# Kernel optimization log

Measured on AMD Instinct MI355X. Metric: run time of the kernel, lower is better.

## Reference

```python
import jax, jax.numpy as jnp
import numpy as np

EPS = 1e-5


def setup_inputs() -> dict:
    key = jax.random.key(0)
    ks = jax.random.split(key, 24)
    B, S, D = 32, 1024, 768        # batch, num_segs, feature_dim
    E, G, C, P = 2, 8, 64, 384     # expansion, groups, num_clusters, latent_clus_dim
    EF = E * D                     # 1536
    GFS = EF // G                  # group_feature_size = 192
    s = 0.02
    f32 = jnp.float32
    return {
        "x": jax.random.normal(ks[0], (B, S, D), f32),
        "W_exp": s * jax.random.normal(ks[1], (D, EF), f32),
        "b_exp": jnp.zeros((EF,), f32),
        "W_ga": s * jax.random.normal(ks[2], (EF, G), f32),
        "b_ga": jnp.zeros((G,), f32),
        "bn1_g": jnp.ones((G * C,), f32) + 0.1 * jax.random.normal(ks[3], (G * C,), f32),
        "bn1_b": 0.1 * jax.random.normal(ks[4], (G * C,), f32),
        "bn1_m": 0.05 * jax.random.normal(ks[5], (G * C,), f32),
        "bn1_v": 1.0 + 0.1 * jax.random.uniform(ks[6], (G * C,), f32),
        "cluster_weights": s * jax.random.normal(ks[7], (EF, G * C), f32),
        "W_proj": s * jax.random.normal(ks[8], (GFS, D), f32),
        "b_proj": jnp.zeros((D,), f32),
        "bn2_g": jnp.ones((C,), f32) + 0.1 * jax.random.normal(ks[9], (C,), f32),
        "bn2_b": 0.1 * jax.random.normal(ks[10], (C,), f32),
        "bn2_m": 0.05 * jax.random.normal(ks[11], (C,), f32),
        "bn2_v": 1.0 + 0.1 * jax.random.uniform(ks[12], (C,), f32),
        "Wq": s * jax.random.normal(ks[13], (D, P), f32),
        "bq": jnp.zeros((P,), f32),
        "Wkv": s * jax.random.normal(ks[14], (D, 2 * P), f32),
        "bkv": jnp.zeros((2 * P,), f32),
        "Wp2": s * jax.random.normal(ks[15], (P, D), f32),
        "bp2": jnp.zeros((D,), f32),
    }


def reference(x, W_exp, b_exp, W_ga, b_ga, bn1_g, bn1_b, bn1_m, bn1_v,
              cluster_weights, W_proj, b_proj, bn2_g, bn2_b, bn2_m, bn2_v,
              Wq, bq, Wkv, bkv, Wp2, bp2):
    B, S, D = x.shape
    EF = W_exp.shape[1]
    G = W_ga.shape[1]
    C = bn2_g.shape[0]
    GFS = EF // G
    P = Wq.shape[1]

    fea = x @ W_exp + b_exp                                   # (B,S,EF)
    ga = jax.nn.sigmoid(fea @ W_ga + b_ga).reshape(B, S * G)  # (B,S*G)

    act = fea.reshape(B * S, EF) @ cluster_weights            # (B*S, G*C)
    act = (act - bn1_m) * (bn1_g / jnp.sqrt(bn1_v + EPS)) + bn1_b  # eval BN
    act = jax.nn.softmax(act.reshape(B, S * G, C), axis=-1) * ga[:, :, None]

    fea_g = fea.reshape(B, S * G, GFS)
    cent = jnp.einsum('bnc,bnf->bcf', act, fea_g)             # (B,C,GFS)

    nc = cent @ W_proj + b_proj                               # (B,C,D)
    scale2 = (bn2_g / jnp.sqrt(bn2_v + EPS))[None, :, None]
    nc = (nc - bn2_m[None, :, None]) * scale2 + bn2_b[None, :, None]

    q = x @ Wq + bq                                           # (B,S,P)
    kv = (nc @ Wkv + bkv).reshape(B, C, 2, P)
    k, v = kv[:, :, 0], kv[:, :, 1]

    scores = jnp.einsum('bsp,bcp->bsc', q, k) / jnp.sqrt(jnp.float32(P))
    attn = jax.nn.softmax(scores, axis=-1)                    # (B,S,C)
    out = jnp.einsum('bsc,bcp->bsp', attn, v)                 # (B,S,P)
    return out @ Wp2 + bp2                                    # (B,S,D)
```

## Files before the change

### kernel.cpp

```cpp
#include <hip/hip_runtime.h>
#include <hip/hip_bf16.h>

#define EPSV 1e-5f

namespace {
constexpr int Bn = 32, Sn = 1024, Dn = 768, Gn = 8, Cn = 64, Pn = 384;
constexpr int EFn = 1536, GFSn = 192, Nrows = Bn * Sn;
}

typedef __attribute__((ext_vector_type(8))) short short8;
typedef __attribute__((ext_vector_type(4))) float f32x4;
typedef __attribute__((ext_vector_type(16))) float f32x16;

__device__ __forceinline__ ushort f2bf(float f) {
  uint u = __builtin_bit_cast(uint, f);
  uint r = (u + 0x7fffu + ((u >> 16) & 1u)) >> 16;
  return (ushort)r;
}
__device__ __forceinline__ uint pack2bf(float lo, float hi) {
  return (uint)f2bf(lo) | ((uint)f2bf(hi) << 16);
}
__device__ __forceinline__ float bf2f(ushort h) {
  return __builtin_bit_cast(float, (uint)h << 16);
}
__device__ __forceinline__ void load16(const ushort* g, ushort* l) {
  __builtin_amdgcn_global_load_lds(
      (const __attribute__((address_space(1))) void*)g,
      (__attribute__((address_space(3))) void*)l, 16, 0, 0);
}
__device__ __forceinline__ int xcd_lid() {
  const int nbx = gridDim.x;
  const int nwg = nbx * gridDim.y;
  const int orig = blockIdx.y * nbx + blockIdx.x;
  const int xq = nwg >> 3, xr = nwg & 7;
  const int xcd = orig & 7, xi = orig >> 3;
  return (xcd < xr ? xcd * (xq + 1) : xr * (xq + 1) + (xcd - xr) * xq) + xi;
}

template <int MODE>
__global__ __launch_bounds__(256) void gemm_bf16(
    const ushort* __restrict__ A, const ushort* __restrict__ BT,
    const float* __restrict__ bias, void* __restrict__ Cout,
    int M, int N, int K,
    const float* __restrict__ g2, const float* __restrict__ b2,
    const float* __restrict__ m2, const float* __restrict__ v2,
    ushort* __restrict__ kq, ushort* __restrict__ vt) {
  __shared__ ushort sh[24576];
  const int tid = threadIdx.x;
  const int wave = tid >> 6, lane = tid & 63;
  const int nbx = gridDim.x;
  const int lid = xcd_lid();
  const int gm = (lid / nbx) * 128, gn = (lid % nbx) * 128;
  const int wr = wave >> 1, wc = wave & 1;

  const int sws = ((tid & 3) ^ ((tid >> 3) & 3)) * 8;
  const int c0 = tid, c1 = tid + 256;
  const ushort* gA0 = A + (size_t)(gm + (c0 >> 2)) * K + sws;
  const ushort* gA1 = A + (size_t)(gm + (c1 >> 2)) * K + sws;
  const ushort* gB0 = BT + (size_t)(gn + (c0 >> 2)) * K + sws;
  const ushort* gB1 = BT + (size_t)(gn + (c1 >> 2)) * K + sws;

  f32x4 acc[4][4] = {};
  const int l15 = lane & 15;
  const int arow = wr * 64 + l15;
  const int brow = wc * 64 + l15;
  const int kswz = (((lane >> 4) ^ ((l15 >> 1) & 3))) * 8;
  const int nk = K >> 5;

#define GB_STAGE(buf, k0)                                    \
  {                                                          \
    load16(gA0 + (k0), &sh[(buf)*8192 + wave * 512]);        \
    load16(gA1 + (k0), &sh[(buf)*8192 + 2048 + wave * 512]); \
    load16(gB0 + (k0), &sh[(buf)*8192 + 4096 + wave * 512]); \
    load16(gB1 + (k0), &sh[(buf)*8192 + 6144 + wave * 512]); \
  }

  GB_STAGE(0, 0);
  GB_STAGE(1, 32);
  int bc = 0;
  for (int t = 0; t < nk; ++t) {
    if (t + 1 < nk) {
      asm volatile("s_waitcnt vmcnt(4)" ::: "memory");
    } else {
      asm volatile("s_waitcnt vmcnt(0)" ::: "memory");
    }
    __builtin_amdgcn_s_barrier();
    __builtin_amdgcn_sched_barrier(0);
    if (t + 2 < nk) {
      const int bp = (bc == 0) ? 2 : bc - 1;
      GB_STAGE(bp, (t + 2) * 32);
    }
    short8 a[4], b[4];
#pragma unroll
    for (int m = 0; m < 4; ++m)
      a[m] = *reinterpret_cast<const short8*>(
          &sh[bc * 8192 + (arow + m * 16) * 32 + kswz]);
#pragma unroll
    for (int n = 0; n < 4; ++n)
      b[n] = *reinterpret_cast<const short8*>(
          &sh[bc * 8192 + 4096 + (brow + n * 16) * 32 + kswz]);
    __builtin_amdgcn_s_setprio(1);
#pragma unroll
    for (int m = 0; m < 4; ++m)
#pragma unroll
      for (int n = 0; n < 4; ++n)
        acc[m][n] = __builtin_amdgcn_mfma_f32_16x16x32_bf16(
            a[m], b[n], acc[m][n], 0, 0, 0);
    __builtin_amdgcn_s_setprio(0);
    __builtin_amdgcn_sched_barrier(0);
    bc = (bc == 2) ? 0 : bc + 1;
  }
#undef GB_STAGE

  const int crow0 = gm + wr * 64 + (lane >> 4) * 4;
  const int ccol0 = gn + wc * 64 + l15;
  float sc_[4][4], sf_[4][4];
  if (MODE == 2) {
#pragma unroll
    for (int m = 0; m < 4; ++m)
#pragma unroll
      for (int j = 0; j < 4; ++j) {
        const int c = (crow0 + m * 16 + j) & 63;
        const float s = g2[c] * rsqrtf(v2[c] + EPSV);
        sc_[m][j] = s;
        sf_[m][j] = b2[c] - m2[c] * s;
      }
  }
#pragma unroll
  for (int m = 0; m < 4; ++m)
#pragma unroll
    for (int n = 0; n < 4; ++n) {
      const int col = ccol0 + n * 16;
      const float bv = bias ? bias[col] : 0.f;
#pragma unroll
      for (int j = 0; j < 4; ++j) {
        const int row = crow0 + m * 16 + j;
        float v = acc[m][n][j] + bv;
        if (MODE == 0) {
          ((float*)Cout)[(size_t)row * N + col] = v;
        } else if (MODE == 1) {
          ((ushort*)Cout)[(size_t)row * N + col] = f2bf(v);
        } else if (MODE == 2) {
          v = v * sc_[m][j] + sf_[m][j];
          ((ushort*)Cout)[(size_t)row * N + col] = f2bf(v);
        } else {
          const ushort h = f2bf(v);
          if (col < 384) {
            kq[(size_t)row * 384 + col] = h;
          } else {
            vt[(size_t)(row >> 6) * 24576 + (size_t)(col - 384) * 64 +
               (row & 63)] = h;
          }
        }
      }
    }
}

__global__ __launch_bounds__(256) void gemm_ga(
    const ushort* __restrict__ fea, const ushort* __restrict__ WTga,
    const float* __restrict__ b_ga, float* __restrict__ ga) {
  constexpr int K = EFn;
  __shared__ ushort sh[13824];
  const int tid = threadIdx.x;
  const int wave = tid >> 6, lane = tid & 63;
  const int gm = blockIdx.x * 128;

  const int sws = ((tid & 3) ^ ((tid >> 3) & 3)) * 8;
  const int swsB = ((lane & 3) ^ ((lane >> 3) & 3)) * 8;
  const int c0 = tid, c1 = tid + 256;
  const ushort* gA0 = fea + (size_t)(gm + (c0 >> 2)) * K + sws;
  const ushort* gA1 = fea + (size_t)(gm + (c1 >> 2)) * K + sws;
  const ushort* gB = WTga + (size_t)(lane >> 2) * K + swsB;

  f32x4 acc[2] = {};
  const int l15 = lane & 15, l4 = lane >> 4;
  const int kswz = ((l4 ^ ((l15 >> 1) & 3))) * 8;
  constexpr int nk = K / 32;

#define GA_STAGE(buf, k0)                                     \
  {                                                           \
    load16(gA0 + (k0), &sh[(buf)*4608 + wave * 512]);         \
    load16(gA1 + (k0), &sh[(buf)*4608 + 2048 + wave * 512]);  \
    if (wave == 0) load16(gB + (k0), &sh[(buf)*4608 + 4096]); \
  }

  GA_STAGE(0, 0);
  GA_STAGE(1, 32);
  int bc = 0;
  for (int t = 0; t < nk; ++t) {
    if (t + 1 < nk) {
      if (wave == 0)
        asm volatile("s_waitcnt vmcnt(3)" ::: "memory");
      else
        asm volatile("s_waitcnt vmcnt(2)" ::: "memory");
    } else {
      asm volatile("s_waitcnt vmcnt(0)" ::: "memory");
    }
    __builtin_amdgcn_s_barrier();
    __builtin_amdgcn_sched_barrier(0);
    if (t + 2 < nk) {
      const int bp = (bc == 0) ? 2 : bc - 1;
      GA_STAGE(bp, (t + 2) * 32);
    }
    const short8 b = *reinterpret_cast<const short8*>(
        &sh[bc * 4608 + 4096 + l15 * 32 + kswz]);
    short8 a[2];
#pragma unroll
    for (int mi = 0; mi < 2; ++mi)
      a[mi] = *reinterpret_cast<const short8*>(
          &sh[bc * 4608 + (wave * 32 + mi * 16 + l15) * 32 + kswz]);
    __builtin_amdgcn_s_setprio(1);
#pragma unroll
    for (int mi = 0; mi < 2; ++mi)
      acc[mi] =
          __builtin_amdgcn_mfma_f32_16x16x32_bf16(a[mi], b, acc[mi], 0, 0, 0);
    __builtin_amdgcn_s_setprio(0);
    __builtin_amdgcn_sched_barrier(0);
    bc = (bc == 2) ? 0 : bc + 1;
  }
#undef GA_STAGE

  if (l15 < 8) {
    const float bv = b_ga[l15];
#pragma unroll
    for (int mi = 0; mi < 2; ++mi)
#pragma unroll
      for (int j = 0; j < 4; ++j) {
        const int row = gm + wave * 32 + mi * 16 + l4 * 4 + j;
        const float v = acc[mi][j] + bv;
        ga[(size_t)row * 8 + l15] = 1.0f / (1.0f + expf(-v));
      }
  }
}

__global__ __launch_bounds__(256) void gemm_sm(
    const ushort* __restrict__ A, const ushort* __restrict__ BT,
    const float* __restrict__ g1, const float* __restrict__ b1,
    const float* __restrict__ m1, const float* __restrict__ v1,
    const float* __restrict__ ga, ushort* __restrict__ actT) {
  constexpr int K = EFn, N = Nrows;
  __shared__ ushort sh[24576];
  __shared__ float sScale[128], sShift[128];
  const int tid = threadIdx.x;
  const int wave = tid >> 6, lane = tid & 63;
  const int lid = xcd_lid();
  const int gm = (lid & 3) * 128;
  const int gn = (lid >> 2) * 128;
  const int wr = wave >> 1, wc = wave & 1;

  if (tid < 128) {
    const int row = gm + tid;
    const float sc = g1[row] * rsqrtf(v1[row] + EPSV);
    sScale[tid] = sc;
    sShift[tid] = b1[row] - m1[row] * sc;
  }

  const int sws = ((tid & 3) ^ ((tid >> 3) & 3)) * 8;
  const int c0 = tid, c1 = tid + 256;
  const ushort* gA0 = A + (size_t)(gm + (c0 >> 2)) * K + sws;
  const ushort* gA1 = A + (size_t)(gm + (c1 >> 2)) * K + sws;
  const ushort* gB0 = BT + (size_t)(gn + (c0 >> 2)) * K + sws;
  const ushort* gB1 = BT + (size_t)(gn + (c1 >> 2)) * K + sws;

  f32x4 acc[4][4] = {};
  const int l15 = lane & 15;
  const int arow = wr * 64 + l15;
  const int brow = wc * 64 + l15;
  const int kswz = (((lane >> 4) ^ ((l15 >> 1) & 3))) * 8;
  constexpr int nk = K >> 5;

#define SM_STAGE(buf, k0)                                    \
  {                                                          \
    load16(gA0 + (k0), &sh[(buf)*8192 + wave * 512]);        \
    load16(gA1 + (k0), &sh[(buf)*8192 + 2048 + wave * 512]); \
    load16(gB0 + (k0), &sh[(buf)*8192 + 4096 + wave * 512]); \
    load16(gB1 + (k0), &sh[(buf)*8192 + 6144 + wave * 512]); \
  }

  SM_STAGE(0, 0);
  SM_STAGE(1, 32);
  int bc = 0;
  for (int t = 0; t < nk; ++t) {
    if (t + 1 < nk) {
      asm volatile("s_waitcnt vmcnt(4)" ::: "memory");
    } else {
      asm volatile("s_waitcnt vmcnt(0)" ::: "memory");
    }
    __builtin_amdgcn_s_barrier();
    __builtin_amdgcn_sched_barrier(0);
    if (t + 2 < nk) {
      const int bp = (bc == 0) ? 2 : bc - 1;
      SM_STAGE(bp, (t + 2) * 32);
    }
    short8 a[4], b[4];
#pragma unroll
    for (int m = 0; m < 4; ++m)
      a[m] = *reinterpret_cast<const short8*>(
          &sh[bc * 8192 + (arow + m * 16) * 32 + kswz]);
#pragma unroll
    for (int n = 0; n < 4; ++n)
      b[n] = *reinterpret_cast<const short8*>(
          &sh[bc * 8192 + 4096 + (brow + n * 16) * 32 + kswz]);
    __builtin_amdgcn_s_setprio(1);
#pragma unroll
    for (int m = 0; m < 4; ++m)
#pragma unroll
      for (int n = 0; n < 4; ++n)
        acc[m][n] = __builtin_amdgcn_mfma_f32_16x16x32_bf16(
            a[m], b[n], acc[m][n], 0, 0, 0);
    __builtin_amdgcn_s_setprio(0);
    __builtin_amdgcn_sched_barrier(0);
    bc = (bc == 2) ? 0 : bc + 1;
  }
#undef SM_STAGE

  const int l4 = lane >> 4;
  const int g = (gm >> 6) + wr;
#pragma unroll
  for (int n = 0; n < 4; ++n) {
    const int col = gn + wc * 64 + n * 16 + l15;
    float mx = -1e30f;
#pragma unroll
    for (int m = 0; m < 4; ++m)
#pragma unroll
      for (int j = 0; j < 4; ++j) {
        const int rl = wr * 64 + m * 16 + l4 * 4 + j;
        acc[m][n][j] = acc[m][n][j] * sScale[rl] + sShift[rl];
        mx = fmaxf(mx, acc[m][n][j]);
      }
    mx = fmaxf(mx, __shfl_xor(mx, 16));
    mx = fmaxf(mx, __shfl_xor(mx, 32));
    float sum = 0.f;
#pragma unroll
    for (int m = 0; m < 4; ++m)
#pragma unroll
      for (int j = 0; j < 4; ++j) {
        acc[m][n][j] = expf(acc[m][n][j] - mx);
        sum += acc[m][n][j];
      }
    sum += __shfl_xor(sum, 16);
    sum += __shfl_xor(sum, 32);
    const float sc = ga[(size_t)col * 8 + g] / sum;
#pragma unroll
    for (int m = 0; m < 4; ++m)
#pragma unroll
      for (int j = 0; j < 4; ++j) {
        const int rowg = gm + wr * 64 + m * 16 + l4 * 4 + j;
        actT[(size_t)rowg * N + col] = f2bf(acc[m][n][j] * sc);
      }
  }
}

__global__ __launch_bounds__(256) void cvt_kernel(const float* __restrict__ in,
                                                  ushort* __restrict__ out,
                                                  int n4) {
  const int i = blockIdx.x * 256 + threadIdx.x;
  if (i >= n4) return;
  const float4 v = reinterpret_cast<const float4*>(in)[i];
  ushort4 o;
  o.x = f2bf(v.x); o.y = f2bf(v.y); o.z = f2bf(v.z); o.w = f2bf(v.w);
  reinterpret_cast<ushort4*>(out)[i] = o;
}

__global__ __launch_bounds__(256) void tconv_kernel(const float* __restrict__ in,
                                                    ushort* __restrict__ out,
                                                    int R, int C) {
  __shared__ float t[32][33];
  const int tx = threadIdx.x & 31, ty = threadIdx.x >> 5;
  const int bc = blockIdx.x * 32, br = blockIdx.y * 32;
#pragma unroll
  for (int i = 0; i < 32; i += 8)
    t[ty + i][tx] = in[(size_t)(br + ty + i) * C + bc + tx];
  __syncthreads();
#pragma unroll
  for (int i = 0; i < 32; i += 8)
    out[(size_t)(bc + ty + i) * R + br + tx] = f2bf(t[tx][ty + i]);
}

__global__ __launch_bounds__(256) void gawt_kernel(const float* __restrict__ in,
                                                   ushort* __restrict__ out) {
  const int k = blockIdx.x * 256 + threadIdx.x;
#pragma unroll
  for (int g = 0; g < 8; ++g) {
    out[(size_t)g * EFn + k] = f2bf(in[(size_t)k * 8 + g]);
    out[(size_t)(g + 8) * EFn + k] = 0;
  }
}

__global__ __launch_bounds__(256) void cent_mfma(
    const ushort* __restrict__ actT, const ushort* __restrict__ fea,
    float* __restrict__ part) {
  __shared__ ushort As[2][64 * 64];
  __shared__ ushort Bs[2][192 * 64];
  const int tid = threadIdx.x;
  const int wave = tid >> 6, lane = tid & 63;
  const int b = blockIdx.x >> 4;
  const int g = (blockIdx.x >> 1) & 7;
  const int ch = blockIdx.x & 1;
  const size_t colbase = (size_t)b * 1024 + ch * 512;
  const int srow = tid >> 2, scp = (tid & 3) * 2;
  const ushort* gA = actT + (size_t)(g * 64 + srow) * Nrows + colbase;
  const int bseg = tid % 24;
  const int bsg = tid / 24;
  const bool bact = tid < 192;
  const ushort* gB =
      fea + (size_t)(colbase + bsg * 8) * EFn + g * 192 + bseg * 8;

  uint4 ra[2], rbv[8];
  f32x4 acc[4][3] = {};
  const int l15 = lane & 15, hi = lane >> 4;
  const int sw = srow & 7;

#define CM_ISSUE(k0)                                                        \
  {                                                                         \
    _Pragma("unroll") for (int i = 0; i < 2; ++i) ra[i] =                   \
        *reinterpret_cast<const uint4*>(gA + (k0) + (scp + i) * 8);         \
    if (bact) {                                                             \
      _Pragma("unroll") for (int i = 0; i < 8; ++i) rbv[i] =                \
          *reinterpret_cast<const uint4*>(gB + (size_t)((k0) + i) * EFn);   \
    }                                                                       \
  }
#define CM_STASH(buf)                                                       \
  {                                                                         \
    _Pragma("unroll") for (int i = 0; i < 2; ++i) {                         \
      const int c = scp + i;                                                \
      *reinterpret_cast<uint4*>(&As[buf][srow * 64 + ((c ^ sw) * 8)]) =     \
          ra[i];                                                            \
    }                                                                       \
    if (bact) {                                                             \
      const ushort* rin = reinterpret_cast<const ushort*>(rbv);             \
      _Pragma("unroll") for (int e = 0; e < 8; ++e) {                       \
        alignas(16) ushort tmp[8];                                          \
        _Pragma("unroll") for (int i = 0; i < 8; ++i) tmp[i] =              \
            rin[i * 8 + e];                                                 \
        const int r = bseg * 8 + e;                                         \
        *reinterpret_cast<uint4*>(&Bs[buf][r * 64 + ((bsg ^ (r & 7)) * 8)]) \
            = *reinterpret_cast<const uint4*>(tmp);                         \
      }                                                                     \
    }                                                                       \
  }

  CM_ISSUE(0);
  CM_STASH(0);
  for (int kk = 0; kk < 8; ++kk) {
    const int buf = kk & 1;
    __syncthreads();
    if (kk < 7) CM_ISSUE((kk + 1) * 64);
#pragma unroll
    for (int ks = 0; ks < 2; ++ks) {
      const int chh = ks * 4 + hi;
      short8 a[4], bb[3];
#pragma unroll
      for (int m = 0; m < 4; ++m) {
        const int r = m * 16 + l15;
        a[m] = *reinterpret_cast<const short8*>(
            &As[buf][r * 64 + ((chh ^ (r & 7)) * 8)]);
      }
#pragma unroll
      for (int nn = 0; nn < 3; ++nn) {
        const int r = wave * 48 + nn * 16 + l15;
        bb[nn] = *reinterpret_cast<const short8*>(
            &Bs[buf][r * 64 + ((chh ^ (r & 7)) * 8)]);
      }
#pragma unroll
      for (int m = 0; m < 4; ++m)
#pragma unroll
        for (int nn = 0; nn < 3; ++nn)
          acc[m][nn] = __builtin_amdgcn_mfma_f32_16x16x32_bf16(
              a[m], bb[nn], acc[m][nn], 0, 0, 0);
    }
    if (kk < 7) CM_STASH(buf ^ 1);
  }
#undef CM_ISSUE
#undef CM_STASH

  float* pb = part + (size_t)blockIdx.x * 12288;
#pragma unroll
  for (int m = 0; m < 4; ++m)
#pragma unroll
    for (int nn = 0; nn < 3; ++nn) {
      const int col = wave * 48 + nn * 16 + l15;
#pragma unroll
      for (int j = 0; j < 4; ++j) {
        const int row = m * 16 + hi * 4 + j;
        pb[row * 192 + col] = acc[m][nn][j];
      }
    }
}

__global__ __launch_bounds__(256) void cent_reduce8(
    const float* __restrict__ part, ushort* __restrict__ cent) {
  const int idx = blockIdx.x * 256 + threadIdx.x;
  const int b = idx / 12288, r = idx % 12288;
  float s = 0.f;
#pragma unroll
  for (int j = 0; j < 16; ++j) s += part[(size_t)(b * 16 + j) * 12288 + r];
  cent[idx] = f2bf(s);
}

__global__ __launch_bounds__(256) void attn_mfma(
    const ushort* __restrict__ qb, const ushort* __restrict__ kb,
    const ushort* __restrict__ vtb, ushort* __restrict__ aout) {
  const int wave = threadIdx.x >> 6, lane = threadIdx.x & 63;
  const int wrow = blockIdx.x * 4 + wave;
  const int row0 = wrow * 32;
  const int b = row0 >> 10;
  const int l31 = lane & 31, hi = lane >> 5;

  f32x16 accs0 = 0.f, accs1 = 0.f;
  const ushort* qp = qb + (size_t)(row0 + l31) * 384 + hi * 8;
  const ushort* kp = kb + (size_t)(b * 64 + l31) * 384 + hi * 8;
#pragma unroll 4
  for (int ks = 0; ks < 24; ++ks) {
    const short8 bq = *reinterpret_cast<const short8*>(qp + ks * 16);
    const short8 a0 = *reinterpret_cast<const short8*>(kp + ks * 16);
    const short8 a1 = *reinterpret_cast<const short8*>(kp + 32 * 384 + ks * 16);
    accs0 = __builtin_amdgcn_mfma_f32_32x32x16_bf16(a0, bq, accs0, 0, 0, 0);
    accs1 = __builtin_amdgcn_mfma_f32_32x32x16_bf16(a1, bq, accs1, 0, 0, 0);
  }

  const float alpha = 0.05103103630798287f;
  float p[32];
#pragma unroll
  for (int i = 0; i < 16; ++i) { p[i] = accs0[i]; p[16 + i] = accs1[i]; }
  float mx = p[0];
#pragma unroll
  for (int i = 1; i < 32; ++i) mx = fmaxf(mx, p[i]);
  mx = fmaxf(mx, __shfl_xor(mx, 32));
  float sum = 0.f;
#pragma unroll
  for (int i = 0; i < 32; ++i) {
    p[i] = expf((p[i] - mx) * alpha);
    sum += p[i];
  }
  sum += __shfl_xor(sum, 32);
  const float inv = 1.0f / sum;

  uint pk0[8], pk1[8];
#pragma unroll
  for (int ct = 0; ct < 2; ++ct)
#pragma unroll
    for (int rg = 0; rg < 4; ++rg) {
      pk0[ct * 4 + rg] =
          pack2bf(p[ct * 16 + rg * 4 + 0] * inv, p[ct * 16 + rg * 4 + 1] * inv);
      pk1[ct * 4 + rg] =
          pack2bf(p[ct * 16 + rg * 4 + 2] * inv, p[ct * 16 + rg * 4 + 3] * inv);
    }
  uint ex0[8], ex1[8];
#pragma unroll
  for (int i = 0; i < 8; ++i) {
    ex0[i] = __shfl_xor(pk0[i], 32);
    ex1[i] = __shfl_xor(pk1[i], 32);
  }

  const ushort* vp = vtb + ((size_t)b * 384 + l31) * 64 + hi * 8;
  ushort* orow = aout + (size_t)(row0 + l31) * 384;
  for (int mt = 0; mt < 12; ++mt) {
    f32x16 acco = 0.f;
#pragma unroll
    for (int kc = 0; kc < 4; ++kc) {
      const short8 av = *reinterpret_cast<const short8*>(
          vp + (size_t)mt * 32 * 64 + kc * 16);
      const int base = (kc >> 1) * 4 + (kc & 1) * 2;
      const uint o0 = hi ? pk0[base + 1] : pk0[base];
      const uint o1 = hi ? pk1[base + 1] : pk1[base];
      const uint e0 = hi ? ex0[base + 1] : ex0[base];
      const uint e1 = hi ? ex1[base + 1] : ex1[base];
      uint4 uu;
      uu.x = hi ? e0 : o0;
      uu.y = hi ? e1 : o1;
      uu.z = hi ? o0 : e0;
      uu.w = hi ? o1 : e1;
      const short8 bp = __builtin_bit_cast(short8, uu);
      acco = __builtin_amdgcn_mfma_f32_32x32x16_bf16(av, bp, acco, 0, 0, 0);
    }
#pragma unroll
    for (int rg = 0; rg < 4; ++rg) {
      ushort4 ov;
      ov.x = f2bf(acco[rg * 4 + 0]);
      ov.y = f2bf(acco[rg * 4 + 1]);
      ov.z = f2bf(acco[rg * 4 + 2]);
      ov.w = f2bf(acco[rg * 4 + 3]);
      *reinterpret_cast<ushort4*>(&orow[mt * 32 + rg * 8 + hi * 4]) = ov;
    }
  }
}

extern "C" void kernel_launch(void* const* d_in, const int* in_sizes, int n_in,
                              void* d_out, int out_size, void* d_ws,
                              size_t ws_size, hipStream_t stream) {
  (void)in_sizes; (void)n_in; (void)out_size; (void)ws_size;
  const float* x      = (const float*)d_in[0];
  const float* W_exp  = (const float*)d_in[1];
  const float* b_exp  = (const float*)d_in[2];
  const float* W_ga   = (const float*)d_in[3];
  const float* b_ga   = (const float*)d_in[4];
  const float* bn1_g  = (const float*)d_in[5];
  const float* bn1_b  = (const float*)d_in[6];
  const float* bn1_m  = (const float*)d_in[7];
  const float* bn1_v  = (const float*)d_in[8];
  const float* cw     = (const float*)d_in[9];
  const float* W_proj = (const float*)d_in[10];
  const float* b_proj = (const float*)d_in[11];
  const float* bn2_g  = (const float*)d_in[12];
  const float* bn2_b  = (const float*)d_in[13];
  const float* bn2_m  = (const float*)d_in[14];
  const float* bn2_v  = (const float*)d_in[15];
  const float* Wq     = (const float*)d_in[16];
  const float* bq     = (const float*)d_in[17];
  const float* Wkv    = (const float*)d_in[18];
  const float* bkv    = (const float*)d_in[19];
  const float* Wp2    = (const float*)d_in[20];
  const float* bp2    = (const float*)d_in[21];
  float* out = (float*)d_out;

  char* ws = (char*)d_ws;
  ushort* fea  = (ushort*)(ws + 0);
  ushort* aout = (ushort*)(ws + 0);
  ushort* xb   = (ushort*)(ws + 100663296ull);
  ushort* actT = (ushort*)(ws + 100663296ull);
  ushort* q_bf = (ushort*)(ws + 150994944ull);
  float*  ga   = (float*)(ws + 176160768ull);
  float*  part = (float*)(ws + 177209344ull);
  ushort* WT1  = (ushort*)(ws + 202375168ull);
  ushort* WT2  = (ushort*)(ws + 204734464ull);
  ushort* WT3  = (ushort*)(ws + 206307328ull);
  ushort* WT4  = (ushort*)(ws + 206897152ull);
  ushort* WT5  = (ushort*)(ws + 207486976ull);
  ushort* WT6  = (ushort*)(ws + 207781888ull);
  ushort* WTga = (ushort*)(ws + 208961536ull);
  ushort* cent = (ushort*)(ws + 209010688ull);
  ushort* nc   = (ushort*)(ws + 209797120ull);
  ushort* k_bf = (ushort*)(ws + 212942848ull);
  ushort* vT_bf= (ushort*)(ws + 214515712ull);

  dim3 blk(256);
  cvt_kernel<<<dim3((Nrows * Dn / 4 + 255) / 256), blk, 0, stream>>>(
      x, xb, Nrows * Dn / 4);
  tconv_kernel<<<dim3(EFn / 32, Dn / 32), blk, 0, stream>>>(W_exp, WT1, Dn, EFn);
  tconv_kernel<<<dim3(512 / 32, EFn / 32), blk, 0, stream>>>(cw, WT2, EFn, 512);
  tconv_kernel<<<dim3(Pn / 32, Dn / 32), blk, 0, stream>>>(Wq, WT3, Dn, Pn);
  tconv_kernel<<<dim3(Dn / 32, Pn / 32), blk, 0, stream>>>(Wp2, WT4, Pn, Dn);
  tconv_kernel<<<dim3(Dn / 32, GFSn / 32), blk, 0, stream>>>(W_proj, WT5, GFSn, Dn);
  tconv_kernel<<<dim3(Dn / 32, Dn / 32), blk, 0, stream>>>(Wkv, WT6, Dn, Dn);
  gawt_kernel<<<dim3(EFn / 256), blk, 0, stream>>>(W_ga, WTga);
  gemm_bf16<1><<<dim3(EFn / 128, Nrows / 128), blk, 0, stream>>>(
      xb, WT1, b_exp, fea, Nrows, EFn, Dn,
      nullptr, nullptr, nullptr, nullptr, nullptr, nullptr);
  gemm_bf16<1><<<dim3(Pn / 128, Nrows / 128), blk, 0, stream>>>(
      xb, WT3, bq, q_bf, Nrows, Pn, Dn,
      nullptr, nullptr, nullptr, nullptr, nullptr, nullptr);
  gemm_ga<<<dim3(Nrows / 128), blk, 0, stream>>>(fea, WTga, b_ga, ga);
  gemm_sm<<<dim3(Nrows / 128, 512 / 128), blk, 0, stream>>>(
      WT2, fea, bn1_g, bn1_b, bn1_m, bn1_v, ga, actT);
  cent_mfma<<<dim3(Bn * Gn * 2), blk, 0, stream>>>(actT, fea, part);
  cent_reduce8<<<dim3(393216 / 256), blk, 0, stream>>>(part, cent);
  gemm_bf16<2><<<dim3(Dn / 128, 2048 / 128), blk, 0, stream>>>(
      cent, WT5, b_proj, nc, 2048, Dn, GFSn,
      bn2_g, bn2_b, bn2_m, bn2_v, nullptr, nullptr);
  gemm_bf16<3><<<dim3(Dn / 128, 2048 / 128), blk, 0, stream>>>(
      nc, WT6, bkv, nullptr, 2048, Dn, Dn,
      nullptr, nullptr, nullptr, nullptr, k_bf, vT_bf);
  attn_mfma<<<dim3(Nrows / 128), blk, 0, stream>>>(q_bf, k_bf, vT_bf, aout);
  gemm_bf16<0><<<dim3(Dn / 128, Nrows / 128), blk, 0, stream>>>(
      aout, WT4, bp2, out, Nrows, Dn, Pn,
      nullptr, nullptr, nullptr, nullptr, nullptr, nullptr);
}
```

Before: 405.7 us.

## Fuse expansion and query GEMMs; add register-B GEMM for output projection

Concatenates the transposed W_exp and Wq weights so a single GEMM over N=1920 writes both fea and q, with epilogue routing by column block and a second bias pointer. This removes one launch and a second pass over xb. The final output projection uses a new gemm_breg kernel that loads B fragments straight from global memory into registers and stages only A in shared memory with triple buffering. This cuts LDS traffic but makes B loads uncoalesced per lane.

```diff
diff --git a/kernel.cpp b/kernel.cpp
--- a/kernel.cpp
+++ b/kernel.cpp
@@ -44,7 +44,8 @@
     int M, int N, int K,
     const float* __restrict__ g2, const float* __restrict__ b2,
     const float* __restrict__ m2, const float* __restrict__ v2,
-    ushort* __restrict__ kq, ushort* __restrict__ vt) {
+    const float* __restrict__ bias2, ushort* __restrict__ kq,
+    ushort* __restrict__ vt) {
   __shared__ ushort sh[24576];
   const int tid = threadIdx.x;
   const int wave = tid >> 6, lane = tid & 63;
@@ -131,19 +132,17 @@
 #pragma unroll
     for (int n = 0; n < 4; ++n) {
       const int col = ccol0 + n * 16;
-      const float bv = bias ? bias[col] : 0.f;
+      const float bv = (MODE == 4)
+                           ? (col < 1536 ? bias[col] : bias2[col - 1536])
+                           : (bias ? bias[col] : 0.f);
 #pragma unroll
       for (int j = 0; j < 4; ++j) {
         const int row = crow0 + m * 16 + j;
         float v = acc[m][n][j] + bv;
-        if (MODE == 0) {
-          ((float*)Cout)[(size_t)row * N + col] = v;
-        } else if (MODE == 1) {
-          ((ushort*)Cout)[(size_t)row * N + col] = f2bf(v);
-        } else if (MODE == 2) {
+        if (MODE == 2) {
           v = v * sc_[m][j] + sf_[m][j];
           ((ushort*)Cout)[(size_t)row * N + col] = f2bf(v);
-        } else {
+        } else if (MODE == 3) {
           const ushort h = f2bf(v);
           if (col < 384) {
             kq[(size_t)row * 384 + col] = h;
@@ -151,8 +150,109 @@
             vt[(size_t)(row >> 6) * 24576 + (size_t)(col - 384) * 64 +
                (row & 63)] = h;
           }
+        } else if (MODE == 4) {
+          const ushort h = f2bf(v);
+          if (gn < 1536)
+            ((ushort*)Cout)[(size_t)row * 1536 + col] = h;
+          else
+            kq[(size_t)row * 384 + (col - 1536)] = h;
         }
       }
+    }
+}
+
+__global__ __launch_bounds__(256) void gemm_breg(
+    const ushort* __restrict__ A, const ushort* __restrict__ BT,
+    const float* __restrict__ bias, float* __restrict__ Cout,
+    int M, int N, int K) {
+  __shared__ ushort sh[12288];
+  const int tid = threadIdx.x;
+  const int wave = tid >> 6, lane = tid & 63;
+  const int nbx = gridDim.x;
+  const int lid = xcd_lid();
+  const int gm = (lid / nbx) * 128, gn = (lid % nbx) * 128;
+  const int wr = wave >> 1, wc = wave & 1;
+
+  const int sws = ((tid & 3) ^ ((tid >> 3) & 3)) * 8;
+  const int c0 = tid, c1 = tid + 256;
+  const ushort* gA0 = A + (size_t)(gm + (c0 >> 2)) * K + sws;
+  const ushort* gA1 = A + (size_t)(gm + (c1 >> 2)) * K + sws;
+
+  f32x4 acc[4][4] = {};
+  const int l15 = lane & 15;
+  const int arow = wr * 64 + l15;
+  const int koff = (lane >> 4) * 8;
+  const ushort* gBr = BT + (size_t)(gn + wc * 64 + l15) * K + koff;
+  const int kswz = (((lane >> 4) ^ ((l15 >> 1) & 3))) * 8;
+  const int nk = K >> 5;
+  int bc = 0;
+
+#define BR_STAGE(buf, k0)                                    \
+  {                                                          \
+    load16(gA0 + (k0), &sh[(buf)*4096 + wave * 512]);        \
+    load16(gA1 + (k0), &sh[(buf)*4096 + 2048 + wave * 512]); \
+  }
+#define BR_LOADB(dst, k0)                                          \
+  {                                                                \
+    _Pragma("unroll") for (int n = 0; n < 4; ++n) dst[n] =         \
+        *reinterpret_cast<const uint4*>(gBr + (size_t)(n * 16) * K \
+                                        + (k0));                   \
+  }
+#define BR_ITER(u, bcur, bnxt)                                        \
+  {                                                                   \
+    if ((u) + 1 < nk)                                                 \
+      asm volatile("s_waitcnt vmcnt(2)" ::: "memory");                \
+    else                                                              \
+      asm volatile("s_waitcnt vmcnt(0)" ::: "memory");                \
+    __builtin_amdgcn_s_barrier();                                     \
+    __builtin_amdgcn_sched_barrier(0);                                \
+    if ((u) + 1 < nk) BR_LOADB(bnxt, ((u) + 1) * 32);                 \
+    __builtin_amdgcn_sched_barrier(0);                                \
+    if ((u) + 2 < nk) {                                               \
+      const int bp = (bc == 0) ? 2 : bc - 1;                          \
+      BR_STAGE(bp, ((u) + 2) * 32);                                   \
+    }                                                                 \
+    __builtin_amdgcn_sched_barrier(0);                                \
+    short8 a[4];                                                      \
+    _Pragma("unroll") for (int m = 0; m < 4; ++m) a[m] =              \
+        *reinterpret_cast<const short8*>(                             \
+            &sh[bc * 4096 + (arow + m * 16) * 32 + kswz]);            \
+    __builtin_amdgcn_s_setprio(1);                                    \
+    _Pragma("unroll") for (int m = 0; m < 4; ++m)                     \
+        _Pragma("unroll") for (int n = 0; n < 4; ++n) acc[m][n] =     \
+            __builtin_amdgcn_mfma_f32_16x16x32_bf16(                  \
+                a[m], __builtin_bit_cast(short8, bcur[n]), acc[m][n], \
+                0, 0, 0);                                             \
+    __builtin_amdgcn_s_setprio(0);                                    \
+    __builtin_amdgcn_sched_barrier(0);                                \
+    bc = (bc == 2) ? 0 : bc + 1;                                      \
+  }
+
+  uint4 b0[4], b1[4];
+  BR_STAGE(0, 0);
+  __builtin_amdgcn_sched_barrier(0);
+  BR_LOADB(b0, 0);
+  __builtin_amdgcn_sched_barrier(0);
+  BR_STAGE(1, 32);
+  for (int t = 0; t < nk; t += 2) {
+    BR_ITER(t, b0, b1);
+    BR_ITER(t + 1, b1, b0);
+  }
+#undef BR_ITER
+#undef BR_LOADB
+#undef BR_STAGE
+
+  const int crow0 = gm + wr * 64 + (lane >> 4) * 4;
+  const int ccol0 = gn + wc * 64 + l15;
+#pragma unroll
+  for (int m = 0; m < 4; ++m)
+#pragma unroll
+    for (int n = 0; n < 4; ++n) {
+      const int col = ccol0 + n * 16;
+      const float bv = bias ? bias[col] : 0.f;
+#pragma unroll
+      for (int j = 0; j < 4; ++j)
+        Cout[(size_t)(crow0 + m * 16 + j) * N + col] = acc[m][n][j] + bv;
     }
 }
 
@@ -615,41 +715,40 @@
   float* out = (float*)d_out;
 
   char* ws = (char*)d_ws;
-  ushort* fea  = (ushort*)(ws + 0);
-  ushort* aout = (ushort*)(ws + 0);
-  ushort* xb   = (ushort*)(ws + 100663296ull);
-  ushort* actT = (ushort*)(ws + 100663296ull);
-  ushort* q_bf = (ushort*)(ws + 150994944ull);
-  float*  ga   = (float*)(ws + 176160768ull);
-  float*  part = (float*)(ws + 177209344ull);
-  ushort* WT1  = (ushort*)(ws + 202375168ull);
-  ushort* WT2  = (ushort*)(ws + 204734464ull);
-  ushort* WT3  = (ushort*)(ws + 206307328ull);
-  ushort* WT4  = (ushort*)(ws + 206897152ull);
-  ushort* WT5  = (ushort*)(ws + 207486976ull);
-  ushort* WT6  = (ushort*)(ws + 207781888ull);
-  ushort* WTga = (ushort*)(ws + 208961536ull);
-  ushort* cent = (ushort*)(ws + 209010688ull);
-  ushort* nc   = (ushort*)(ws + 209797120ull);
-  ushort* k_bf = (ushort*)(ws + 212942848ull);
-  ushort* vT_bf= (ushort*)(ws + 214515712ull);
+  ushort* fea   = (ushort*)(ws + 0);
+  ushort* aout  = (ushort*)(ws + 0);
+  ushort* xb    = (ushort*)(ws + 100663296ull);
+  ushort* actT  = (ushort*)(ws + 100663296ull);
+  ushort* q_bf  = (ushort*)(ws + 150994944ull);
+  float*  ga    = (float*)(ws + 176160768ull);
+  float*  part  = (float*)(ws + 177209344ull);
+  ushort* WTcat = (ushort*)(ws + 202375168ull);
+  ushort* WT2   = (ushort*)(ws + 205324288ull);
+  ushort* WT4   = (ushort*)(ws + 206897152ull);
+  ushort* WT5   = (ushort*)(ws + 207486976ull);
+  ushort* WT6   = (ushort*)(ws + 207781888ull);
+  ushort* WTga  = (ushort*)(ws + 208961536ull);
+  ushort* cent  = (ushort*)(ws + 209010688ull);
+  ushort* nc    = (ushort*)(ws + 209797120ull);
+  ushort* k_bf  = (ushort*)(ws + 212942848ull);
+  ushort* vT_bf = (ushort*)(ws + 214515712ull);
 
   dim3 blk(256);
   cvt_kernel<<<dim3((Nrows * Dn / 4 + 255) / 256), blk, 0, stream>>>(
       x, xb, Nrows * Dn / 4);
-  tconv_kernel<<<dim3(EFn / 32, Dn / 32), blk, 0, stream>>>(W_exp, WT1, Dn, EFn);
+  tconv_kernel<<<dim3(EFn / 32, Dn / 32), blk, 0, stream>>>(W_exp, WTcat, Dn,
+                                                            EFn);
+  tconv_kernel<<<dim3(Pn / 32, Dn / 32), blk, 0, stream>>>(
+      Wq, WTcat + (size_t)1536 * 768, Dn, Pn);
   tconv_kernel<<<dim3(512 / 32, EFn / 32), blk, 0, stream>>>(cw, WT2, EFn, 512);
-  tconv_kernel<<<dim3(Pn / 32, Dn / 32), blk, 0, stream>>>(Wq, WT3, Dn, Pn);
   tconv_kernel<<<dim3(Dn / 32, Pn / 32), blk, 0, stream>>>(Wp2, WT4, Pn, Dn);
-  tconv_kernel<<<dim3(Dn / 32, GFSn / 32), blk, 0, stream>>>(W_proj, WT5, GFSn, Dn);
+  tconv_kernel<<<dim3(Dn / 32, GFSn / 32), blk, 0, stream>>>(W_proj, WT5, GFSn,
+                                                             Dn);
   tconv_kernel<<<dim3(Dn / 32, Dn / 32), blk, 0, stream>>>(Wkv, WT6, Dn, Dn);
   gawt_kernel<<<dim3(EFn / 256), blk, 0, stream>>>(W_ga, WTga);
-  gemm_bf16<1><<<dim3(EFn / 128, Nrows / 128), blk, 0, stream>>>(
-      xb, WT1, b_exp, fea, Nrows, EFn, Dn,
-      nullptr, nullptr, nullptr, nullptr, nullptr, nullptr);
-  gemm_bf16<1><<<dim3(Pn / 128, Nrows / 128), blk, 0, stream>>>(
-      xb, WT3, bq, q_bf, Nrows, Pn, Dn,
-      nullptr, nullptr, nullptr, nullptr, nullptr, nullptr);
+  gemm_bf16<4><<<dim3(1920 / 128, Nrows / 128), blk, 0, stream>>>(
+      xb, WTcat, b_exp, fea, Nrows, 1920, Dn,
+      nullptr, nullptr, nullptr, nullptr, bq, q_bf, nullptr);
   gemm_ga<<<dim3(Nrows / 128), blk, 0, stream>>>(fea, WTga, b_ga, ga);
   gemm_sm<<<dim3(Nrows / 128, 512 / 128), blk, 0, stream>>>(
       WT2, fea, bn1_g, bn1_b, bn1_m, bn1_v, ga, actT);
@@ -657,12 +756,11 @@
   cent_reduce8<<<dim3(393216 / 256), blk, 0, stream>>>(part, cent);
   gemm_bf16<2><<<dim3(Dn / 128, 2048 / 128), blk, 0, stream>>>(
       cent, WT5, b_proj, nc, 2048, Dn, GFSn,
-      bn2_g, bn2_b, bn2_m, bn2_v, nullptr, nullptr);
+      bn2_g, bn2_b, bn2_m, bn2_v, nullptr, nullptr, nullptr);
   gemm_bf16<3><<<dim3(Dn / 128, 2048 / 128), blk, 0, stream>>>(
       nc, WT6, bkv, nullptr, 2048, Dn, Dn,
-      nullptr, nullptr, nullptr, nullptr, k_bf, vT_bf);
+      nullptr, nullptr, nullptr, nullptr, nullptr, k_bf, vT_bf);
   attn_mfma<<<dim3(Nrows / 128), blk, 0, stream>>>(q_bf, k_bf, vT_bf, aout);
-  gemm_bf16<0><<<dim3(Dn / 128, Nrows / 128), blk, 0, stream>>>(
-      aout, WT4, bp2, out, Nrows, Dn, Pn,
-      nullptr, nullptr, nullptr, nullptr, nullptr, nullptr);
-}
+  gemm_breg<<<dim3(Dn / 128, Nrows / 128), blk, 0, stream>>>(
+      aout, WT4, bp2, out, Nrows, Dn, Pn);
+}
```

Result: no change. 413.4 us (+1.9%).
